# Optimization experiments

Measured on AMD Instinct MI355X. Metric: run time of the kernel, lower is better.

## Reference

```python
import jax, jax.numpy as jnp
import numpy as np

EPSILON = 1e-36


def setup_inputs() -> dict:
    key = jax.random.key(0)
    k1, k2, k3, k4 = jax.random.split(key, 4)
    n, in_dim, out_dim = 8192, 128, 128
    x = jax.random.normal(k1, (n, in_dim), dtype=jnp.float32)
    # xavier-uniform-like scale for W_real
    limit = float(np.sqrt(6.0 / (in_dim + out_dim)))
    W_real = jax.random.uniform(k2, (in_dim, out_dim), dtype=jnp.float32, minval=-limit, maxval=limit)
    W_imag = jax.random.uniform(k3, (in_dim, out_dim), dtype=jnp.float32, minval=-0.1, maxval=0.1)
    G = jax.random.uniform(k4, (in_dim, out_dim), dtype=jnp.float32, minval=0.0, maxval=1.0)
    return {"x": x, "W_real": W_real, "W_imag": W_imag, "G": G}


def reference(x, W_real, W_imag, G):
    Gc = jnp.clip(G, 0.0, 1.0)                                   # (i,o)
    # R: (n,i,o) = |x| gated toward 1 by (1-G)
    R = (jnp.abs(x) + EPSILON)[:, :, None] * Gc[None] + (1.0 - Gc)[None]
    # K: pi where x<0, gated by G
    K = jnp.pi * (x < 0).astype(x.dtype)[:, :, None] * Gc[None]  # (n,i,o)
    logR = jnp.log(R)
    A = jnp.einsum('nio,io->no', logR, W_real) - jnp.einsum('nio,io->no', K, W_imag)
    B = jnp.einsum('nio,io->no', logR, W_imag) + jnp.einsum('nio,io->no', K, W_real)
    return jnp.exp(A) * jnp.cos(B)
```

## Files before the change

kernel.cpp:

```cpp
#include <hip/hip_runtime.h>
#include <math.h>


#define NROWS 8192
#define DIM   128
#define RPB   8
#define NT    512
#define PI_F  3.14159265358979323846f
#define LN2_F 0.69314718055994530942f

typedef float v2f __attribute__((ext_vector_type(2)));

static __device__ __forceinline__ v2f vfma2(v2f a, v2f b, v2f c) {
    return __builtin_elementwise_fma(a, b, c);
}

__global__ __launch_bounds__(256) void prep(
    const float* __restrict__ Wr, const float* __restrict__ Wi,
    const float* __restrict__ G,
    float4* __restrict__ wq, float2* __restrict__ wb)
{
    int t = blockIdx.x * 256 + threadIdx.x;
    if (t < DIM * DIM) {
        float g  = fminf(fmaxf(G[t], 0.0f), 1.0f);
        float wr = Wr[t], wi = Wi[t];
        wq[t] = make_float4(LN2_F * wr, LN2_F * wi, g, 1.0f - g);
        wb[t] = make_float2(-PI_F * g * wi, PI_F * g * wr);
    }
}

__global__ __launch_bounds__(NT, 8) void main_kernel(
    const float* __restrict__ x, const float4* __restrict__ wq,
    const float2* __restrict__ wb, float* __restrict__ out)
{
    __shared__ float2 P[8][RPB][64];

    const int tid   = threadIdx.x;
    const int lane  = tid & 63;
    const int w     = tid >> 6;
    const int h     = w & 1;
    const int iq    = w >> 1;
    const int i0    = iq * 32;
    const int nbase = blockIdx.x * RPB;
    const int o     = h * 64 + lane;

    float vx[4];
#pragma unroll
    for (int k = 0; k < 4; ++k)
        vx[k] = x[(size_t)(nbase + 2 * k + (lane >> 5)) * DIM + i0 + (lane & 31)];

    v2f acc[RPB];
#pragma unroll
    for (int r = 0; r < RPB; ++r) acc[r] = (v2f){0.f, 0.f};

    const float4* wqp = wq + (size_t)i0 * DIM + o;
    const float2* wbp = wb + (size_t)i0 * DIM + o;

    float4 wqc = wqp[0];
    float2 wbc = wbp[0];

#pragma unroll 2
    for (int ii = 0; ii < 32; ++ii) {
        const int nx = (ii + 1) & 31;
        float4 wqn = wqp[(size_t)nx * DIM];
        float2 wbn = wbp[(size_t)nx * DIM];

        const float g  = wqc.z;
        const float hh = wqc.w;
        const v2f   w2  = {wqc.x, wqc.y};
        const v2f   pg2 = {wbc.x, wbc.y};

#pragma unroll
        for (int r = 0; r < RPB; ++r) {
            int   xi = __builtin_amdgcn_readlane(__float_as_int(vx[r >> 1]),
                                                 (r & 1) * 32 + ii);
            float xr = __int_as_float(xi);
            float ax = fabsf(xr);
            float sf = (xr < 0.0f) ? 1.0f : 0.0f;
            float t  = fmaf(g, ax, hh);
            float l  = __log2f(t);
            acc[r] = vfma2((v2f){l, l}, w2,
                           vfma2((v2f){sf, sf}, pg2, acc[r]));
        }
        wqc = wqn; wbc = wbn;
    }

#pragma unroll
    for (int r = 0; r < RPB; ++r)
        P[w][r][lane] = make_float2(acc[r].x, acc[r].y);
    __syncthreads();

#pragma unroll
    for (int cc = 0; cc < 2; ++cc) {
        const int c  = tid + cc * NT;
        const int r  = c >> 7;
        const int oo = c & (DIM - 1);
        const int h2 = oo >> 6, ol = oo & 63;
        float A = 0.f, B = 0.f;
#pragma unroll
        for (int q2 = 0; q2 < 4; ++q2) {
            float2 p = P[q2 * 2 + h2][r][ol];
            A += p.x; B += p.y;
        }
        out[(size_t)(nbase + r) * DIM + oo] = __expf(A) * __cosf(B);
    }
}

__global__ __launch_bounds__(NT, 4) void fb_kernel(
    const float* __restrict__ x,
    const float* __restrict__ Wr, const float* __restrict__ Wi,
    const float* __restrict__ G, float* __restrict__ out)
{
    __shared__ float sbuf[4 * RPB * DIM];
    float* am1p = sbuf;
    float* psp  = sbuf + DIM * RPB;

    const int tid   = threadIdx.x;
    const int o     = tid & (DIM - 1);
    const int q     = tid >> 7;
    const int nbase = blockIdx.x * RPB;

    {
        const float* xb = x + (size_t)nbase * DIM;
        float2 v = ((const float2*)xb)[tid];
        int e = tid * 2;
        int i = e & (DIM - 1), r = e >> 7;
        am1p[i * RPB + r]       = fabsf(v.x) - 1.0f;
        am1p[(i + 1) * RPB + r] = fabsf(v.y) - 1.0f;
        psp[i * RPB + r]        = (v.x < 0.0f) ? PI_F : 0.0f;
        psp[(i + 1) * RPB + r]  = (v.y < 0.0f) ? PI_F : 0.0f;
    }
    __syncthreads();

    v2f accA[4], accB[4];
#pragma unroll
    for (int p = 0; p < 4; ++p) { accA[p] = (v2f){0.f, 0.f}; accB[p] = (v2f){0.f, 0.f}; }

    const int ibase = q * 32;
#pragma unroll 4
    for (int ii = 0; ii < 32; ++ii) {
        const int i = ibase + ii;
        const int wi_idx = i * DIM + o;
        float g   = fminf(fmaxf(G[wi_idx], 0.0f), 1.0f);
        float wrl = LN2_F * Wr[wi_idx];
        float wil = LN2_F * Wi[wi_idx];
        const float ngwi = -g * (wil * (1.0f / LN2_F));
        const float gwr  =  g * (wrl * (1.0f / LN2_F));
        const v2f gg2 = {g, g}, wrl2 = {wrl, wrl}, wil2 = {wil, wil};
        const v2f ngwi2 = {ngwi, ngwi}, gwr2 = {gwr, gwr}, one2 = {1.f, 1.f};

        const float4* a4 = (const float4*)(am1p + i * RPB);
        const float4* p4 = (const float4*)(psp  + i * RPB);
        float4 a03 = a4[0], a47 = a4[1];
        float4 s03 = p4[0], s47 = p4[1];

#define ROWPAIR(mx, my, sx, sy, idx)                                        \
        do {                                                                \
            v2f t2 = vfma2((v2f){mx, my}, gg2, one2);                       \
            v2f l2 = { __log2f(t2.x), __log2f(t2.y) };                      \
            v2f s2 = {sx, sy};                                              \
            accA[idx] = vfma2(l2, wrl2, vfma2(s2, ngwi2, accA[idx]));       \
            accB[idx] = vfma2(l2, wil2, vfma2(s2, gwr2,  accB[idx]));       \
        } while (0)

        ROWPAIR(a03.x, a03.y, s03.x, s03.y, 0);
        ROWPAIR(a03.z, a03.w, s03.z, s03.w, 1);
        ROWPAIR(a47.x, a47.y, s47.x, s47.y, 2);
        ROWPAIR(a47.z, a47.w, s47.z, s47.w, 3);
#undef ROWPAIR
    }

    float* pP = sbuf;
    const int c = tid * 2;
    const int r = c >> 7, oo = c & (DIM - 1);

    __syncthreads();
#pragma unroll
    for (int p = 0; p < 4; ++p) {
        pP[q * (RPB * DIM) + (2 * p) * DIM + o]     = accA[p].x;
        pP[q * (RPB * DIM) + (2 * p + 1) * DIM + o] = accA[p].y;
    }
    __syncthreads();
    v2f A = {0.f, 0.f};
#pragma unroll
    for (int qq = 0; qq < 4; ++qq)
        A += *(const v2f*)&pP[qq * (RPB * DIM) + r * DIM + oo];
    __syncthreads();
#pragma unroll
    for (int p = 0; p < 4; ++p) {
        pP[q * (RPB * DIM) + (2 * p) * DIM + o]     = accB[p].x;
        pP[q * (RPB * DIM) + (2 * p + 1) * DIM + o] = accB[p].y;
    }
    __syncthreads();
    v2f B = {0.f, 0.f};
#pragma unroll
    for (int qq = 0; qq < 4; ++qq)
        B += *(const v2f*)&pP[qq * (RPB * DIM) + r * DIM + oo];

    float2 res;
    res.x = __expf(A.x) * __cosf(B.x);
    res.y = __expf(A.y) * __cosf(B.y);
    *(float2*)&out[(size_t)(nbase + r) * DIM + oo] = res;
}

extern "C" void kernel_launch(void* const* d_in, const int* in_sizes, int n_in,
                              void* d_out, int out_size, void* d_ws, size_t ws_size,
                              hipStream_t stream) {
    const float* x  = (const float*)d_in[0];
    const float* Wr = (const float*)d_in[1];
    const float* Wi = (const float*)d_in[2];
    const float* G  = (const float*)d_in[3];
    float* out = (float*)d_out;

    const size_t wq_bytes = (size_t)DIM * DIM * sizeof(float4);
    const size_t wb_bytes = (size_t)DIM * DIM * sizeof(float2);
    if (ws_size >= wq_bytes + wb_bytes) {
        float4* wq = (float4*)d_ws;
        float2* wb = (float2*)((char*)d_ws + wq_bytes);
        prep<<<(DIM * DIM + 255) / 256, 256, 0, stream>>>(Wr, Wi, G, wq, wb);
        main_kernel<<<NROWS / RPB, NT, 0, stream>>>(x, wq, wb, out);
    } else {
        fb_kernel<<<NROWS / RPB, NT, 0, stream>>>(x, Wr, Wi, G, out);
    }
}
```

Before: 98.79 us.

## Process 16 rows per block with LDS-staged inputs and split A/B accumulators

Doubles rows per block in the main kernel so each weight-table load from cache is amortized over twice as many rows. Inputs are staged in shared memory as |x|-1 and a sign flag instead of being broadcast via readlane. Weights are prefetched two iterations ahead, and outputs are stored as float4. The cost is more registers and fewer resident blocks (launch bound occupancy drops from 8 to 4).

```diff
diff --git a/kernel.cpp b/kernel.cpp
--- a/kernel.cpp
+++ b/kernel.cpp
@@ -4,7 +4,7 @@
 
 #define NROWS 8192
 #define DIM   128
-#define RPB   8
+#define RPB   16
 #define NT    512
 #define PI_F  3.14159265358979323846f
 #define LN2_F 0.69314718055994530942f
@@ -24,16 +24,18 @@
     if (t < DIM * DIM) {
         float g  = fminf(fmaxf(G[t], 0.0f), 1.0f);
         float wr = Wr[t], wi = Wi[t];
-        wq[t] = make_float4(LN2_F * wr, LN2_F * wi, g, 1.0f - g);
+        wq[t] = make_float4(LN2_F * wr, LN2_F * wi, g, 0.0f);
         wb[t] = make_float2(-PI_F * g * wi, PI_F * g * wr);
     }
 }
 
-__global__ __launch_bounds__(NT, 8) void main_kernel(
+__global__ __launch_bounds__(NT, 4) void main_kernel(
     const float* __restrict__ x, const float4* __restrict__ wq,
     const float2* __restrict__ wb, float* __restrict__ out)
 {
-    __shared__ float2 P[8][RPB][64];
+    __shared__ float sbuf[4 * RPB * DIM];
+    float* am1p = sbuf;
+    float* sfp  = sbuf + DIM * RPB;
 
     const int tid   = threadIdx.x;
     const int lane  = tid & 63;
@@ -41,69 +43,114 @@
     const int h     = w & 1;
     const int iq    = w >> 1;
     const int i0    = iq * 32;
+    const int o     = h * 64 + lane;
     const int nbase = blockIdx.x * RPB;
-    const int o     = h * 64 + lane;
-
-    float vx[4];
-#pragma unroll
-    for (int k = 0; k < 4; ++k)
-        vx[k] = x[(size_t)(nbase + 2 * k + (lane >> 5)) * DIM + i0 + (lane & 31)];
-
-    v2f acc[RPB];
-#pragma unroll
-    for (int r = 0; r < RPB; ++r) acc[r] = (v2f){0.f, 0.f};
+
+    {
+        const float4* xb = (const float4*)(x + (size_t)nbase * DIM);
+        float4 v = xb[tid];
+        int e = tid * 4;
+        int i = e & (DIM - 1), r = e >> 7;
+        float vv[4] = {v.x, v.y, v.z, v.w};
+#pragma unroll
+        for (int k = 0; k < 4; ++k) {
+            am1p[(i + k) * RPB + r] = fabsf(vv[k]) - 1.0f;
+            sfp[(i + k) * RPB + r]  = (vv[k] < 0.0f) ? 1.0f : 0.0f;
+        }
+    }
+    __syncthreads();
+
+    v2f accA[8], accB[8];
+#pragma unroll
+    for (int p = 0; p < 8; ++p) { accA[p] = (v2f){0.f, 0.f}; accB[p] = (v2f){0.f, 0.f}; }
 
     const float4* wqp = wq + (size_t)i0 * DIM + o;
     const float2* wbp = wb + (size_t)i0 * DIM + o;
 
-    float4 wqc = wqp[0];
-    float2 wbc = wbp[0];
+    float4 wq0 = wqp[0],   wq1 = wqp[DIM];
+    float2 wb0 = wbp[0],   wb1 = wbp[DIM];
 
 #pragma unroll 2
     for (int ii = 0; ii < 32; ++ii) {
-        const int nx = (ii + 1) & 31;
-        float4 wqn = wqp[(size_t)nx * DIM];
-        float2 wbn = wbp[(size_t)nx * DIM];
-
-        const float g  = wqc.z;
-        const float hh = wqc.w;
-        const v2f   w2  = {wqc.x, wqc.y};
-        const v2f   pg2 = {wbc.x, wbc.y};
-
-#pragma unroll
-        for (int r = 0; r < RPB; ++r) {
-            int   xi = __builtin_amdgcn_readlane(__float_as_int(vx[r >> 1]),
-                                                 (r & 1) * 32 + ii);
-            float xr = __int_as_float(xi);
-            float ax = fabsf(xr);
-            float sf = (xr < 0.0f) ? 1.0f : 0.0f;
-            float t  = fmaf(g, ax, hh);
-            float l  = __log2f(t);
-            acc[r] = vfma2((v2f){l, l}, w2,
-                           vfma2((v2f){sf, sf}, pg2, acc[r]));
-        }
-        wqc = wqn; wbc = wbn;
-    }
-
-#pragma unroll
-    for (int r = 0; r < RPB; ++r)
-        P[w][r][lane] = make_float2(acc[r].x, acc[r].y);
-    __syncthreads();
-
-#pragma unroll
-    for (int cc = 0; cc < 2; ++cc) {
-        const int c  = tid + cc * NT;
-        const int r  = c >> 7;
-        const int oo = c & (DIM - 1);
-        const int h2 = oo >> 6, ol = oo & 63;
-        float A = 0.f, B = 0.f;
-#pragma unroll
-        for (int q2 = 0; q2 < 4; ++q2) {
-            float2 p = P[q2 * 2 + h2][r][ol];
-            A += p.x; B += p.y;
-        }
-        out[(size_t)(nbase + r) * DIM + oo] = __expf(A) * __cosf(B);
-    }
+        const int p2 = (ii + 2) & 31;
+        float4 wqn = wqp[(size_t)p2 * DIM];
+        float2 wbn = wbp[(size_t)p2 * DIM];
+
+        const int i = i0 + ii;
+        const float4* a4 = (const float4*)(am1p + i * RPB);
+        const float4* s4 = (const float4*)(sfp  + i * RPB);
+        float4 aA = a4[0], aB = a4[1], aC = a4[2], aD = a4[3];
+        float4 sA = s4[0], sB = s4[1], sC = s4[2], sD = s4[3];
+
+        const float g    = wq0.z;
+        const float wrl  = wq0.x, wil = wq0.y;
+        const float ngwi = wb0.x, pgwr = wb0.y;
+        const v2f gg2   = {g, g};
+        const v2f wrl2  = {wrl, wrl};
+        const v2f wil2  = {wil, wil};
+        const v2f ngwi2 = {ngwi, ngwi};
+        const v2f pgwr2 = {pgwr, pgwr};
+        const v2f one2  = {1.0f, 1.0f};
+
+#define ROWPAIR(mx, my, sx, sy, idx)                                        \
+        do {                                                                \
+            v2f t2 = vfma2((v2f){mx, my}, gg2, one2);                       \
+            v2f l2 = { __log2f(t2.x), __log2f(t2.y) };                      \
+            v2f s2 = {sx, sy};                                              \
+            accA[idx] = vfma2(l2, wrl2, vfma2(s2, ngwi2, accA[idx]));       \
+            accB[idx] = vfma2(l2, wil2, vfma2(s2, pgwr2, accB[idx]));       \
+        } while (0)
+
+        ROWPAIR(aA.x, aA.y, sA.x, sA.y, 0);
+        ROWPAIR(aA.z, aA.w, sA.z, sA.w, 1);
+        ROWPAIR(aB.x, aB.y, sB.x, sB.y, 2);
+        ROWPAIR(aB.z, aB.w, sB.z, sB.w, 3);
+        ROWPAIR(aC.x, aC.y, sC.x, sC.y, 4);
+        ROWPAIR(aC.z, aC.w, sC.z, sC.w, 5);
+        ROWPAIR(aD.x, aD.y, sD.x, sD.y, 6);
+        ROWPAIR(aD.z, aD.w, sD.z, sD.w, 7);
+#undef ROWPAIR
+
+        wq0 = wq1; wq1 = wqn;
+        wb0 = wb1; wb1 = wbn;
+    }
+
+    float* pP = sbuf;
+    const int c4 = tid * 4;
+
+    __syncthreads();
+#pragma unroll
+    for (int p = 0; p < 8; ++p) {
+        pP[iq * (RPB * DIM) + (2 * p) * DIM + o]     = accA[p].x;
+        pP[iq * (RPB * DIM) + (2 * p + 1) * DIM + o] = accA[p].y;
+    }
+    __syncthreads();
+    float4 A4 = make_float4(0.f, 0.f, 0.f, 0.f);
+#pragma unroll
+    for (int q2 = 0; q2 < 4; ++q2) {
+        float4 t = *(const float4*)&pP[q2 * (RPB * DIM) + c4];
+        A4.x += t.x; A4.y += t.y; A4.z += t.z; A4.w += t.w;
+    }
+    __syncthreads();
+#pragma unroll
+    for (int p = 0; p < 8; ++p) {
+        pP[iq * (RPB * DIM) + (2 * p) * DIM + o]     = accB[p].x;
+        pP[iq * (RPB * DIM) + (2 * p + 1) * DIM + o] = accB[p].y;
+    }
+    __syncthreads();
+    float4 B4 = make_float4(0.f, 0.f, 0.f, 0.f);
+#pragma unroll
+    for (int q2 = 0; q2 < 4; ++q2) {
+        float4 t = *(const float4*)&pP[q2 * (RPB * DIM) + c4];
+        B4.x += t.x; B4.y += t.y; B4.z += t.z; B4.w += t.w;
+    }
+
+    float4 res;
+    res.x = __expf(A4.x) * __cosf(B4.x);
+    res.y = __expf(A4.y) * __cosf(B4.y);
+    res.z = __expf(A4.z) * __cosf(B4.z);
+    res.w = __expf(A4.w) * __cosf(B4.w);
+    ((float4*)(out + (size_t)nbase * DIM))[tid] = res;
 }
 
 __global__ __launch_bounds__(NT, 4) void fb_kernel(
@@ -111,24 +158,24 @@
     const float* __restrict__ Wr, const float* __restrict__ Wi,
     const float* __restrict__ G, float* __restrict__ out)
 {
-    __shared__ float sbuf[4 * RPB * DIM];
+    __shared__ float sbuf[4 * 8 * DIM];
     float* am1p = sbuf;
-    float* psp  = sbuf + DIM * RPB;
+    float* psp  = sbuf + DIM * 8;
 
     const int tid   = threadIdx.x;
     const int o     = tid & (DIM - 1);
     const int q     = tid >> 7;
-    const int nbase = blockIdx.x * RPB;
+    const int nbase = blockIdx.x * 8;
 
     {
         const float* xb = x + (size_t)nbase * DIM;
         float2 v = ((const float2*)xb)[tid];
         int e = tid * 2;
         int i = e & (DIM - 1), r = e >> 7;
-        am1p[i * RPB + r]       = fabsf(v.x) - 1.0f;
-        am1p[(i + 1) * RPB + r] = fabsf(v.y) - 1.0f;
-        psp[i * RPB + r]        = (v.x < 0.0f) ? PI_F : 0.0f;
-        psp[(i + 1) * RPB + r]  = (v.y < 0.0f) ? PI_F : 0.0f;
+        am1p[i * 8 + r]       = fabsf(v.x) - 1.0f;
+        am1p[(i + 1) * 8 + r] = fabsf(v.y) - 1.0f;
+        psp[i * 8 + r]        = (v.x < 0.0f) ? PI_F : 0.0f;
+        psp[(i + 1) * 8 + r]  = (v.y < 0.0f) ? PI_F : 0.0f;
     }
     __syncthreads();
 
@@ -149,8 +196,8 @@
         const v2f gg2 = {g, g}, wrl2 = {wrl, wrl}, wil2 = {wil, wil};
         const v2f ngwi2 = {ngwi, ngwi}, gwr2 = {gwr, gwr}, one2 = {1.f, 1.f};
 
-        const float4* a4 = (const float4*)(am1p + i * RPB);
-        const float4* p4 = (const float4*)(psp  + i * RPB);
+        const float4* a4 = (const float4*)(am1p + i * 8);
+        const float4* p4 = (const float4*)(psp  + i * 8);
         float4 a03 = a4[0], a47 = a4[1];
         float4 s03 = p4[0], s47 = p4[1];
 
@@ -177,25 +224,25 @@
     __syncthreads();
 #pragma unroll
     for (int p = 0; p < 4; ++p) {
-        pP[q * (RPB * DIM) + (2 * p) * DIM + o]     = accA[p].x;
-        pP[q * (RPB * DIM) + (2 * p + 1) * DIM + o] = accA[p].y;
+        pP[q * (8 * DIM) + (2 * p) * DIM + o]     = accA[p].x;
+        pP[q * (8 * DIM) + (2 * p + 1) * DIM + o] = accA[p].y;
     }
     __syncthreads();
     v2f A = {0.f, 0.f};
 #pragma unroll
     for (int qq = 0; qq < 4; ++qq)
-        A += *(const v2f*)&pP[qq * (RPB * DIM) + r * DIM + oo];
+        A += *(const v2f*)&pP[qq * (8 * DIM) + r * DIM + oo];
     __syncthreads();
 #pragma unroll
     for (int p = 0; p < 4; ++p) {
-        pP[q * (RPB * DIM) + (2 * p) * DIM + o]     = accB[p].x;
-        pP[q * (RPB * DIM) + (2 * p + 1) * DIM + o] = accB[p].y;
+        pP[q * (8 * DIM) + (2 * p) * DIM + o]     = accB[p].x;
+        pP[q * (8 * DIM) + (2 * p + 1) * DIM + o] = accB[p].y;
     }
     __syncthreads();
     v2f B = {0.f, 0.f};
 #pragma unroll
     for (int qq = 0; qq < 4; ++qq)
-        B += *(const v2f*)&pP[qq * (RPB * DIM) + r * DIM + oo];
+        B += *(const v2f*)&pP[qq * (8 * DIM) + r * DIM + oo];
 
     float2 res;
     res.x = __expf(A.x) * __cosf(B.x);
@@ -220,6 +267,6 @@
         prep<<<(DIM * DIM + 255) / 256, 256, 0, stream>>>(Wr, Wi, G, wq, wb);
         main_kernel<<<NROWS / RPB, NT, 0, stream>>>(x, wq, wb, out);
     } else {
-        fb_kernel<<<NROWS / RPB, NT, 0, stream>>>(x, Wr, Wi, G, out);
-    }
-}
+        fb_kernel<<<NROWS / 8, NT, 0, stream>>>(x, Wr, Wi, G, out);
+    }
+}
```

New measurement: 88.26 us. -10.7%, faster.
